# Optimization experiments

Hardware: AMD Instinct MI355X
Metric: run time of the kernel (lower is better)

The kernel has to match this reference:

```python
import jax, jax.numpy as jnp
import numpy as np

B, S, D, H, F = 2, 2048, 1024, 16, 4096
HD = D // H
EPS = 1e-5
NEG = -1e9


def _layernorm(x, g, b):
    mu = jnp.mean(x, axis=-1, keepdims=True)
    var = jnp.mean((x - mu) ** 2, axis=-1, keepdims=True)
    return (x - mu) * jax.lax.rsqrt(var + EPS) * g + b


def _attention(x, wq, wk, wv, wo, bo):
    b, s, d = x.shape
    q = (x @ wq).reshape(b, s, H, HD).transpose(0, 2, 1, 3)  # [b,h,s,hd]
    k = (x @ wk).reshape(b, s, H, HD).transpose(0, 2, 1, 3)
    v = (x @ wv).reshape(b, s, H, HD).transpose(0, 2, 1, 3)
    scores = jnp.einsum('bhqd,bhkd->bhqk', q, k) / (HD ** 0.5)
    # Faithful to source bug: masked_fill(mask == 0, -1e9) where mask = triu(diag=1)
    # -> positions with k <= q (lower triangle incl. diagonal) are filled with -1e9.
    lower = jnp.tril(jnp.ones((s, s), dtype=bool))
    scores = jnp.where(lower, NEG, scores)
    w = jax.nn.softmax(scores, axis=-1)
    o = jnp.einsum('bhqk,bhkd->bhqd', w, v)
    o = o.transpose(0, 2, 1, 3).reshape(b, s, d)
    return o @ wo + bo


def _ffn(x, w1, b1, w2, b2):
    return jax.nn.gelu(x @ w1 + b1, approximate=False) @ w2 + b2


def setup_inputs() -> dict:
    key = jax.random.key(0)
    ks = jax.random.split(key, 10)
    s = 0.02
    return {
        'x': jax.random.normal(ks[0], (B, S, D), jnp.float32),
        'wq': jax.random.normal(ks[1], (D, D), jnp.float32) * s,
        'wk': jax.random.normal(ks[2], (D, D), jnp.float32) * s,
        'wv': jax.random.normal(ks[3], (D, D), jnp.float32) * s,
        'wo': jax.random.normal(ks[4], (D, D), jnp.float32) * s,
        'bo': jnp.zeros((D,), jnp.float32),
        'ln1_g': jnp.ones((D,), jnp.float32),
        'ln1_b': jnp.zeros((D,), jnp.float32),
        'ln2_g': jnp.ones((D,), jnp.float32),
        'ln2_b': jnp.zeros((D,), jnp.float32),
        'w1': jax.random.normal(ks[5], (D, F), jnp.float32) * s,
        'b1': jnp.zeros((F,), jnp.float32),
        'w2': jax.random.normal(ks[6], (F, D), jnp.float32) * s,
        'b2': jnp.zeros((D,), jnp.float32),
    }


def reference(x, wq, wk, wv, wo, bo, ln1_g, ln1_b, ln2_g, ln2_b, w1, b1, w2, b2):
    shortcut = x
    h = _layernorm(x, ln1_g, ln1_b)
    h = _attention(h, wq, wk, wv, wo, bo)  # dropout = identity (eval)
    h = h + shortcut
    shortcut = h
    h2 = _layernorm(h, ln2_g, ln2_b)
    h2 = _attention(h2, wq, wk, wv, wo, bo)  # same attn module reused, per source
    h2 = _ffn(h2, w1, b1, w2, b2)
    return h2 + shortcut
```

## Files before the change

### kernel.cpp

```cpp
#include <hip/hip_runtime.h>
#include <hip/hip_bf16.h>
#include <math.h>

#define Bz 2
#define Sz 2048
#define Dz 1024
#define Hz 16
#define HDz 64
#define Fz 4096
#define ROWS (Bz*Sz)
#define EPSf 1e-5f
#define NEGf -1e9f

typedef __attribute__((ext_vector_type(8))) short short8;
typedef __attribute__((ext_vector_type(4))) float floatx4;

__device__ __forceinline__ unsigned short f2bf(float f){
  __hip_bfloat16 h = __float2bfloat16(f);
  return *(unsigned short*)&h;
}
__device__ __forceinline__ float bf2f(unsigned short u){
  union { unsigned x; float f; } a; a.x = ((unsigned)u) << 16; return a.f;
}

__device__ __forceinline__ float fast_gelu(float x){
  float t  = fabsf(x) * 0.70710678118654752f;
  float kk = __builtin_amdgcn_rcpf(1.0f + 0.3275911f * t);
  float poly = ((((1.061405429f*kk - 1.453152027f)*kk + 1.421413741f)*kk
                 - 0.284496736f)*kk + 0.254829592f)*kk;
  float er = 1.0f - poly * __expf(-t*t);
  er = copysignf(er, x);
  return 0.5f * x * (1.0f + er);
}

__device__ __forceinline__ void gload16(const void* g, void* l){
  __builtin_amdgcn_global_load_lds(
      (const __attribute__((address_space(1))) unsigned int*)g,
      (__attribute__((address_space(3))) unsigned int*)l, 16, 0, 0);
}

__device__ __forceinline__ void xcd_remap(int& bmblk, int& bnblk){
  int gx = gridDim.x, gy = gridDim.y;
  int id = blockIdx.y * gx + blockIdx.x;
  int xcd = id & 7, local = id >> 3;
  bnblk = local % gx;
  bmblk = xcd * (gy >> 3) + local / gx;
}

__global__ __launch_bounds__(256)
void transpose_cast(const float* __restrict__ W, unsigned short* __restrict__ Wt,
                    int K, int N)
{
  __shared__ unsigned short Ts[32][33];
  int n0 = blockIdx.x*32, k0 = blockIdx.y*32;
  int r = threadIdx.x >> 3, c0 = (threadIdx.x & 7) * 4;
  float4 w4 = *(const float4*)(W + (size_t)(k0+r)*N + n0 + c0);
  Ts[r][c0+0] = f2bf(w4.x); Ts[r][c0+1] = f2bf(w4.y);
  Ts[r][c0+2] = f2bf(w4.z); Ts[r][c0+3] = f2bf(w4.w);
  __syncthreads();
  unsigned v0 = Ts[c0+0][r], v1 = Ts[c0+1][r], v2 = Ts[c0+2][r], v3 = Ts[c0+3][r];
  uint2 p; p.x = v0 | (v1<<16); p.y = v2 | (v3<<16);
  *(uint2*)(Wt + (size_t)(n0+r)*K + k0 + c0) = p;
}

__global__ __launch_bounds__(256)
void ln_kernel(const float* __restrict__ in, const float* __restrict__ gam,
               const float* __restrict__ bet, unsigned short* __restrict__ out)
{
  int row = blockIdx.x, t = threadIdx.x;
  size_t base = (size_t)row * Dz;
  int c0 = t * 4;
  float4 x4 = *(const float4*)(in + base + c0);
  float v[4] = {x4.x, x4.y, x4.z, x4.w};
  float s = v[0]+v[1]+v[2]+v[3];
  #pragma unroll
  for (int off=32; off>0; off>>=1) s += __shfl_down(s, off, 64);
  __shared__ float ws[4];
  int lane = t & 63, wid = t >> 6;
  if (lane == 0) ws[wid] = s;
  __syncthreads();
  float mu = (ws[0]+ws[1]+ws[2]+ws[3]) * (1.0f/Dz);
  __syncthreads();
  float d0=v[0]-mu, d1=v[1]-mu, d2=v[2]-mu, d3=v[3]-mu;
  float s2 = d0*d0+d1*d1+d2*d2+d3*d3;
  #pragma unroll
  for (int off=32; off>0; off>>=1) s2 += __shfl_down(s2, off, 64);
  if (lane == 0) ws[wid] = s2;
  __syncthreads();
  float var = (ws[0]+ws[1]+ws[2]+ws[3]) * (1.0f/Dz);
  float rstd = rsqrtf(var + EPSf);
  float4 g4 = *(const float4*)(gam + c0);
  float4 b4 = *(const float4*)(bet + c0);
  unsigned r0 = f2bf((v[0]-mu)*rstd*g4.x + b4.x);
  unsigned r1 = f2bf((v[1]-mu)*rstd*g4.y + b4.y);
  unsigned r2 = f2bf((v[2]-mu)*rstd*g4.z + b4.z);
  unsigned r3 = f2bf((v[3]-mu)*rstd*g4.w + b4.w);
  uint2 p; p.x = r0 | (r1<<16); p.y = r2 | (r3<<16);
  *(uint2*)(out + base + c0) = p;
}

__global__ __launch_bounds__(256)
void gemm_mfma(const unsigned short* __restrict__ A,
               const unsigned short* __restrict__ Bt,
               const float* __restrict__ bias, const float* __restrict__ res,
               float* __restrict__ outf, unsigned short* __restrict__ outb,
               int M, int N, int K, int act, int qkvmode)
{
  __shared__ unsigned short As[2][128*32];
  __shared__ unsigned short Bs[2][128*32];
  int t = threadIdx.x;
  int bmblk, bnblk; xcd_remap(bmblk, bnblk);
  int bm = bmblk * 128, bn = bnblk * 128;
  int wave = t >> 6, lane = t & 63;
  int l15 = lane & 15, quad = lane >> 4;
  int wm = (wave & 1) * 64, wn = (wave >> 1) * 64;
  int srow = wave*32 + (lane >> 2);
  int scbg = ((lane & 3) ^ ((lane >> 3) & 3)) * 8;
  const unsigned short* gA = A  + (size_t)(bm + srow)*K + scbg;
  const unsigned short* gB = Bt + (size_t)(bn + srow)*K + scbg;

  floatx4 acc[4][4];
  #pragma unroll
  for (int i=0;i<4;i++)
    #pragma unroll
    for (int j=0;j<4;j++) acc[i][j] = (floatx4){0.f,0.f,0.f,0.f};

  int swa = ((l15 >> 1) & 3);

  {
    unsigned short* lA = &As[0][wave*32*32];
    unsigned short* lB = &Bs[0][wave*32*32];
    gload16(gA,                lA);
    gload16(gA + (size_t)16*K, lA + 16*32);
    gload16(gB,                lB);
    gload16(gB + (size_t)16*K, lB + 16*32);
  }

  int nIter = K >> 5;
  for (int it = 0; it < nIter; ++it) {
    __syncthreads();
    int cur = it & 1;
    if (it + 1 < nIter) {
      int k1 = (it+1) << 5;
      unsigned short* lA = &As[cur^1][wave*32*32];
      unsigned short* lB = &Bs[cur^1][wave*32*32];
      gload16(gA + k1,                lA);
      gload16(gA + k1 + (size_t)16*K, lA + 16*32);
      gload16(gB + k1,                lB);
      gload16(gB + k1 + (size_t)16*K, lB + 16*32);
    }
    const unsigned short* Ac = As[cur];
    const unsigned short* Bc = Bs[cur];
    short8 af[4], bf[4];
    #pragma unroll
    for (int i=0;i<4;i++) af[i] = *(const short8*)&Ac[(wm + i*16 + l15)*32 + (quad ^ swa)*8];
    #pragma unroll
    for (int j=0;j<4;j++) bf[j] = *(const short8*)&Bc[(wn + j*16 + l15)*32 + (quad ^ swa)*8];
    #pragma unroll
    for (int i=0;i<4;i++)
      #pragma unroll
      for (int j=0;j<4;j++)
        acc[i][j] = __builtin_amdgcn_mfma_f32_16x16x32_bf16(af[i], bf[j], acc[i][j], 0, 0, 0);
  }

  float bj[4];
  #pragma unroll
  for (int j=0;j<4;j++) bj[j] = bias ? bias[bn + wn + j*16 + l15] : 0.f;

  size_t selbase = 0; int ncol = N;
  if (qkvmode) { selbase = (size_t)(bn >> 10) * ((size_t)ROWS * 1024); ncol = 1024; }
  int bnl = qkvmode ? (bn & 1023) : bn;

  #pragma unroll
  for (int i=0;i<4;i++){
    int row0 = bm + wm + i*16 + quad*4;
    #pragma unroll
    for (int r=0;r<4;r++){
      size_t rowoff = selbase + (size_t)(row0 + r) * ncol;
      #pragma unroll
      for (int j=0;j<4;j++){
        float v = acc[i][j][r] + bj[j];
        if (act) v = fast_gelu(v);
        size_t off = rowoff + bnl + wn + j*16 + l15;
        if (res) v += res[off];
        if (outf) outf[off] = v;
        else      outb[off] = f2bf(v);
      }
    }
  }
}

__global__ __launch_bounds__(256)
void gemm_n64(const unsigned short* __restrict__ A,
              const unsigned short* __restrict__ Bt,
              const float* __restrict__ bias, const float* __restrict__ res,
              float* __restrict__ outf, unsigned short* __restrict__ outb,
              int M, int N, int K)
{
  __shared__ unsigned short As[2][128*64];
  __shared__ unsigned short Bs[2][64*64];
  int t = threadIdx.x;
  int bmblk, bnblk; xcd_remap(bmblk, bnblk);
  int bm = bmblk * 128, bn = bnblk * 64;
  int wave = t >> 6, lane = t & 63;
  int l15 = lane & 15, quad = lane >> 4;
  int arow = lane >> 3;
  int acbg = ((lane & 7) ^ arow) * 8;
  const unsigned short* gA = A  + (size_t)(bm + wave*32 + arow)*K + acbg;
  const unsigned short* gB = Bt + (size_t)(bn + wave*16 + arow)*K + acbg;

  floatx4 acc[2][4];
  #pragma unroll
  for (int i=0;i<2;i++)
    #pragma unroll
    for (int j=0;j<4;j++) acc[i][j] = (floatx4){0.f,0.f,0.f,0.f};

  int swr = (l15 & 7);

  {
    unsigned short* lA = &As[0][wave*32*64];
    unsigned short* lB = &Bs[0][wave*16*64];
    gload16(gA,                 lA);
    gload16(gA + (size_t)8*K,   lA + 8*64);
    gload16(gA + (size_t)16*K,  lA + 16*64);
    gload16(gA + (size_t)24*K,  lA + 24*64);
    gload16(gB,                 lB);
    gload16(gB + (size_t)8*K,   lB + 8*64);
  }

  int nIter = K >> 6;
  for (int it = 0; it < nIter; ++it) {
    __syncthreads();
    int cur = it & 1;
    if (it + 1 < nIter) {
      int k1 = (it+1) << 6;
      unsigned short* lA = &As[cur^1][wave*32*64];
      unsigned short* lB = &Bs[cur^1][wave*16*64];
      gload16(gA + k1,                 lA);
      gload16(gA + k1 + (size_t)8*K,   lA + 8*64);
      gload16(gA + k1 + (size_t)16*K,  lA + 16*64);
      gload16(gA + k1 + (size_t)24*K,  lA + 24*64);
      gload16(gB + k1,                 lB);
      gload16(gB + k1 + (size_t)8*K,   lB + 8*64);
    }
    const unsigned short* Ac = As[cur];
    const unsigned short* Bc = Bs[cur];
    #pragma unroll
    for (int ks=0; ks<2; ++ks){
      short8 af[2], bf[4];
      #pragma unroll
      for (int i=0;i<2;i++)
        af[i] = *(const short8*)&Ac[(wave*32 + i*16 + l15)*64 + ((ks*4 + quad) ^ swr)*8];
      #pragma unroll
      for (int j=0;j<4;j++)
        bf[j] = *(const short8*)&Bc[(j*16 + l15)*64 + ((ks*4 + quad) ^ swr)*8];
      #pragma unroll
      for (int i=0;i<2;i++)
        #pragma unroll
        for (int j=0;j<4;j++)
          acc[i][j] = __builtin_amdgcn_mfma_f32_16x16x32_bf16(af[i], bf[j], acc[i][j], 0, 0, 0);
    }
  }

  float bj[4];
  #pragma unroll
  for (int j=0;j<4;j++) bj[j] = bias ? bias[bn + j*16 + l15] : 0.f;

  #pragma unroll
  for (int i=0;i<2;i++){
    int row0 = bm + wave*32 + i*16 + quad*4;
    #pragma unroll
    for (int r=0;r<4;r++){
      size_t rowoff = (size_t)(row0 + r) * N;
      #pragma unroll
      for (int j=0;j<4;j++){
        float v = acc[i][j][r] + bj[j];
        size_t off = rowoff + bn + j*16 + l15;
        if (res) v += res[off];
        if (outf) outf[off] = v;
        else      outb[off] = f2bf(v);
      }
    }
  }
}

__global__ __launch_bounds__(256)
void vmean_kernel(const unsigned short* __restrict__ v, float* __restrict__ vm)
{
  int h = blockIdx.x, b = blockIdx.y;
  int t = threadIdx.x, d = t & 63, seg = t >> 6;
  float s = 0.f;
  for (int i=0;i<512;i++){
    int srow = seg*512 + i;
    s += bf2f(v[((size_t)(b*Sz + srow))*Dz + h*HDz + d]);
  }
  __shared__ float red[4][64];
  red[seg][d] = s;
  __syncthreads();
  if (seg == 0){
    float tot = red[0][d]+red[1][d]+red[2][d]+red[3][d];
    vm[(b*Hz + h)*HDz + d] = tot * (1.0f/2048.0f);
  }
}

__global__ __launch_bounds__(256)
void attn_mfma(const unsigned short* __restrict__ Qg,
               const unsigned short* __restrict__ Kg,
               const unsigned short* __restrict__ Vg,
               const float* __restrict__ vmean,
               unsigned short* __restrict__ Og)
{
  __shared__ unsigned short Ks[128][72];
  __shared__ unsigned short Vts[64][136];
  __shared__ unsigned short Ps[128][72];

  int t = threadIdx.x;
  int wave = t >> 6, lane = t & 63;
  int l15 = lane & 15, quad = lane >> 4;
  int b = blockIdx.z, h = blockIdx.y;
  int qt = b ? (15 - (int)blockIdx.x) : (int)blockIdx.x;

  {
    int r = t >> 1, c = (t & 1) * 32;
    const unsigned short* qp = Qg + ((size_t)(b*Sz + qt*128 + r))*Dz + h*HDz + c;
    uint4 q0 = *(const uint4*)(qp);
    uint4 q1 = *(const uint4*)(qp + 8);
    uint4 q2 = *(const uint4*)(qp + 16);
    uint4 q3 = *(const uint4*)(qp + 24);
    *(uint4*)&Ps[r][c]      = q0;
    *(uint4*)&Ps[r][c + 8]  = q1;
    *(uint4*)&Ps[r][c + 16] = q2;
    *(uint4*)&Ps[r][c + 24] = q3;
  }
  __syncthreads();
  short8 aq[2][2];
  #pragma unroll
  for (int i=0;i<2;i++)
    #pragma unroll
    for (int ks=0;ks<2;ks++)
      aq[i][ks] = *(const short8*)&Ps[wave*32 + i*16 + l15][ks*32 + quad*8];

  floatx4 acc_o[2][4];
  #pragma unroll
  for (int i=0;i<2;i++)
    #pragma unroll
    for (int j=0;j<4;j++) acc_o[i][j] = (floatx4){0.f,0.f,0.f,0.f};
  float lacc[2][4];
  #pragma unroll
  for (int i=0;i<2;i++)
    #pragma unroll
    for (int r=0;r<4;r++) lacc[i][r] = 0.f;

  int sr = t >> 2, sc = (t & 3) * 16;

  uint4 pk0,pk1,pk2,pk3,pv0,pv1,pv2,pv3;
  {
    size_t off0 = ((size_t)(b*Sz + qt*128 + sr))*Dz + h*HDz + sc;
    size_t off1 = off0 + (size_t)64*Dz;
    pk0 = *(const uint4*)(Kg + off0); pk1 = *(const uint4*)(Kg + off0 + 8);
    pk2 = *(const uint4*)(Kg + off1); pk3 = *(const uint4*)(Kg + off1 + 8);
    pv0 = *(const uint4*)(Vg + off0); pv1 = *(const uint4*)(Vg + off0 + 8);
    pv2 = *(const uint4*)(Vg + off1); pv3 = *(const uint4*)(Vg + off1 + 8);
  }

  for (int jt2 = qt; jt2 < Sz/128; ++jt2) {
    __syncthreads();
    {
      *(uint4*)&Ks[sr][sc]        = pk0; *(uint4*)&Ks[sr][sc + 8]      = pk1;
      *(uint4*)&Ks[64 + sr][sc]   = pk2; *(uint4*)&Ks[64 + sr][sc + 8] = pk3;
      unsigned short e[16];
      e[0]=pv0.x&0xffff; e[1]=pv0.x>>16; e[2]=pv0.y&0xffff; e[3]=pv0.y>>16;
      e[4]=pv0.z&0xffff; e[5]=pv0.z>>16; e[6]=pv0.w&0xffff; e[7]=pv0.w>>16;
      e[8]=pv1.x&0xffff; e[9]=pv1.x>>16; e[10]=pv1.y&0xffff; e[11]=pv1.y>>16;
      e[12]=pv1.z&0xffff; e[13]=pv1.z>>16; e[14]=pv1.w&0xffff; e[15]=pv1.w>>16;
      #pragma unroll
      for (int j=0;j<16;j++) Vts[sc + j][sr] = e[j];
      e[0]=pv2.x&0xffff; e[1]=pv2.x>>16; e[2]=pv2.y&0xffff; e[3]=pv2.y>>16;
      e[4]=pv2.z&0xffff; e[5]=pv2.z>>16; e[6]=pv2.w&0xffff; e[7]=pv2.w>>16;
      e[8]=pv3.x&0xffff; e[9]=pv3.x>>16; e[10]=pv3.y&0xffff; e[11]=pv3.y>>16;
      e[12]=pv3.z&0xffff; e[13]=pv3.z>>16; e[14]=pv3.w&0xffff; e[15]=pv3.w>>16;
      #pragma unroll
      for (int j=0;j<16;j++) Vts[sc + j][64 + sr] = e[j];
    }
    __syncthreads();

    if (jt2 + 1 < Sz/128) {
      size_t off0 = ((size_t)(b*Sz + (jt2+1)*128 + sr))*Dz + h*HDz + sc;
      size_t off1 = off0 + (size_t)64*Dz;
      pk0 = *(const uint4*)(Kg + off0); pk1 = *(const uint4*)(Kg + off0 + 8);
      pk2 = *(const uint4*)(Kg + off1); pk3 = *(const uint4*)(Kg + off1 + 8);
      pv0 = *(const uint4*)(Vg + off0); pv1 = *(const uint4*)(Vg + off0 + 8);
      pv2 = *(const uint4*)(Vg + off1); pv3 = *(const uint4*)(Vg + off1 + 8);
    }

    #pragma unroll
    for (int hh=0; hh<2; ++hh){
      floatx4 acc_s[2][4];
      #pragma unroll
      for (int i=0;i<2;i++)
        #pragma unroll
        for (int j=0;j<4;j++) acc_s[i][j] = (floatx4){0.f,0.f,0.f,0.f};
      #pragma unroll
      for (int ks=0;ks<2;ks++){
        short8 bk[4];
        #pragma unroll
        for (int j=0;j<4;j++) bk[j] = *(const short8*)&Ks[hh*64 + j*16 + l15][ks*32 + quad*8];
        #pragma unroll
        for (int i=0;i<2;i++)
          #pragma unroll
          for (int j=0;j<4;j++)
            acc_s[i][j] = __builtin_amdgcn_mfma_f32_16x16x32_bf16(aq[i][ks], bk[j], acc_s[i][j], 0, 0, 0);
      }
      #pragma unroll
      for (int i=0;i<2;i++){
        #pragma unroll
        for (int j=0;j<4;j++){
          int kj = jt2*128 + hh*64 + j*16 + l15;
          #pragma unroll
          for (int r=0;r<4;r++){
            int qrow = qt*128 + wave*32 + i*16 + quad*4 + r;
            float s = acc_s[i][j][r] * 0.125f;
            if (kj <= qrow) s = NEGf;
            float p = __expf(fminf(s, 80.f));
            lacc[i][r] += p;
            Ps[wave*32 + i*16 + quad*4 + r][j*16 + l15] = f2bf(p);
          }
        }
      }
      #pragma unroll
      for (int ks=0;ks<2;ks++){
        short8 ap[2], bv[4];
        #pragma unroll
        for (int i=0;i<2;i++) ap[i] = *(const short8*)&Ps[wave*32 + i*16 + l15][ks*32 + quad*8];
        #pragma unroll
        for (int j=0;j<4;j++) bv[j] = *(const short8*)&Vts[j*16 + l15][hh*64 + ks*32 + quad*8];
        #pragma unroll
        for (int i=0;i<2;i++)
          #pragma unroll
          for (int j=0;j<4;j++)
            acc_o[i][j] = __builtin_amdgcn_mfma_f32_16x16x32_bf16(ap[i], bv[j], acc_o[i][j], 0, 0, 0);
      }
    }
  }

  #pragma unroll
  for (int i=0;i<2;i++){
    #pragma unroll
    for (int r=0;r<4;r++){
      float l = lacc[i][r];
      l += __shfl_xor(l, 1, 64);
      l += __shfl_xor(l, 2, 64);
      l += __shfl_xor(l, 4, 64);
      l += __shfl_xor(l, 8, 64);
      int qrow = qt*128 + wave*32 + i*16 + quad*4 + r;
      float inv = 1.0f / l;
      size_t rowoff = ((size_t)(b*Sz + qrow))*Dz + h*HDz;
      #pragma unroll
      for (int j=0;j<4;j++){
        float ov = acc_o[i][j][r] * inv;
        if (qrow == Sz-1) ov = vmean[(b*Hz + h)*HDz + j*16 + l15];
        Og[rowoff + j*16 + l15] = f2bf(ov);
      }
    }
  }
}

extern "C" void kernel_launch(void* const* d_in, const int* in_sizes, int n_in,
                              void* d_out, int out_size, void* d_ws, size_t ws_size,
                              hipStream_t stream)
{
  const float* x    = (const float*)d_in[0];
  const float* wq   = (const float*)d_in[1];
  const float* wk   = (const float*)d_in[2];
  const float* wv   = (const float*)d_in[3];
  const float* wo   = (const float*)d_in[4];
  const float* bo   = (const float*)d_in[5];
  const float* ln1g = (const float*)d_in[6];
  const float* ln1b = (const float*)d_in[7];
  const float* ln2g = (const float*)d_in[8];
  const float* ln2b = (const float*)d_in[9];
  const float* w1   = (const float*)d_in[10];
  const float* b1   = (const float*)d_in[11];
  const float* w2   = (const float*)d_in[12];
  const float* b2   = (const float*)d_in[13];
  float* out = (float*)d_out;

  const size_t MB = 1024*1024;
  char* w = (char*)d_ws;
  float*          trunk = (float*)(w);
  unsigned short* lnb   = (unsigned short*)(w + 16*MB);
  float*          vmean = (float*)(w + 16*MB);
  unsigned short* q     = (unsigned short*)(w + 24*MB);
  unsigned short* k     = (unsigned short*)(w + 32*MB);
  unsigned short* v     = (unsigned short*)(w + 40*MB);
  unsigned short* ctx   = (unsigned short*)(w + 48*MB);
  unsigned short* wqkvT = (unsigned short*)(w + 56*MB);
  unsigned short* wqT   = wqkvT;
  unsigned short* wkT   = (unsigned short*)(w + 58*MB);
  unsigned short* wvT   = (unsigned short*)(w + 60*MB);
  unsigned short* woT   = (unsigned short*)(w + 62*MB);
  unsigned short* w1T   = (unsigned short*)(w + 64*MB);
  unsigned short* w2T   = (unsigned short*)(w + 72*MB);
  unsigned short* mid   = (unsigned short*)(w + 24*MB);

  dim3 blk(256);
  transpose_cast<<<dim3(32,32),  blk, 0, stream>>>(wq, wqT, Dz, Dz);
  transpose_cast<<<dim3(32,32),  blk, 0, stream>>>(wk, wkT, Dz, Dz);
  transpose_cast<<<dim3(32,32),  blk, 0, stream>>>(wv, wvT, Dz, Dz);
  transpose_cast<<<dim3(32,32),  blk, 0, stream>>>(wo, woT, Dz, Dz);
  transpose_cast<<<dim3(128,32), blk, 0, stream>>>(w1, w1T, Dz, Fz);
  transpose_cast<<<dim3(32,128), blk, 0, stream>>>(w2, w2T, Fz, Dz);

  dim3 gln(ROWS);
  dim3 gqkv(3*Dz/128, ROWS/128);
  dim3 gn64(Dz/64,  ROWS/128);
  dim3 gf1(Fz/128, ROWS/128);
  dim3 gattn(Sz/128, Hz, Bz);
  dim3 gvm(Hz, Bz);

  ln_kernel<<<gln, blk, 0, stream>>>(x, ln1g, ln1b, lnb);
  gemm_mfma<<<gqkv, blk, 0, stream>>>(lnb, wqkvT, nullptr, nullptr, nullptr, q, ROWS, 3*Dz, Dz, 0, 1);
  vmean_kernel<<<gvm, blk, 0, stream>>>(v, vmean);
  attn_mfma<<<gattn, blk, 0, stream>>>(q, k, v, vmean, ctx);
  gemm_n64<<<gn64, blk, 0, stream>>>(ctx, woT, bo, x, trunk, nullptr, ROWS, Dz, Dz);

  ln_kernel<<<gln, blk, 0, stream>>>(trunk, ln2g, ln2b, lnb);
  gemm_mfma<<<gqkv, blk, 0, stream>>>(lnb, wqkvT, nullptr, nullptr, nullptr, q, ROWS, 3*Dz, Dz, 0, 1);
  vmean_kernel<<<gvm, blk, 0, stream>>>(v, vmean);
  attn_mfma<<<gattn, blk, 0, stream>>>(q, k, v, vmean, ctx);
  gemm_n64<<<gn64, blk, 0, stream>>>(ctx, woT, bo, nullptr, nullptr, lnb, ROWS, Dz, Dz);
  gemm_mfma<<<gf1, blk, 0, stream>>>(lnb, w1T, b1, nullptr, nullptr, mid, ROWS, Fz, Dz, 1, 0);
  gemm_n64<<<gn64, blk, 0, stream>>>(mid, w2T, b2, trunk, out, nullptr, ROWS, Dz, Fz);
}
```

Baseline: 531.8 us.

## Replace 128x128 GEMM with 256x256 8-wave pipelined kernel and split-K FFN2

Replaces the 128x128 bf16 MFMA GEMM with a 256x256-tile, 512-thread kernel that uses a K-tile of 64, XOR-swizzled LDS, and an interleaved schedule of staged loads, barriers and prioritized MFMA phases. It is used for the QKV and FFN1 projections. When the workspace is large enough, FFN2 runs as a 4-way split-K with this kernel, followed by a reduction kernel that adds bias and residual. The aim is more operand reuse per tile and better overlap of loads with MFMA work, at the cost of fewer blocks (possible wave quantization), higher register pressure, and extra memory traffic for the split-K partials.

```diff
diff --git a/kernel.cpp b/kernel.cpp
--- a/kernel.cpp
+++ b/kernel.cpp
@@ -38,6 +38,15 @@
       (const __attribute__((address_space(1))) unsigned int*)g,
       (__attribute__((address_space(3))) unsigned int*)l, 16, 0, 0);
 }
+
+__device__ __forceinline__ void bar(){
+  asm volatile("" ::: "memory");
+  __builtin_amdgcn_s_barrier();
+  asm volatile("" ::: "memory");
+}
+#define WAITV6 asm volatile("s_waitcnt vmcnt(6)" ::: "memory")
+#define WAITV0 asm volatile("s_waitcnt vmcnt(0)" ::: "memory")
+#define WL0    asm volatile("s_waitcnt lgkmcnt(0)" ::: "memory")
 
 __device__ __forceinline__ void xcd_remap(int& bmblk, int& bnblk){
   int gx = gridDim.x, gy = gridDim.y;
@@ -99,81 +108,176 @@
   *(uint2*)(out + base + c0) = p;
 }
 
-__global__ __launch_bounds__(256)
-void gemm_mfma(const unsigned short* __restrict__ A,
-               const unsigned short* __restrict__ Bt,
-               const float* __restrict__ bias, const float* __restrict__ res,
-               float* __restrict__ outf, unsigned short* __restrict__ outb,
-               int M, int N, int K, int act, int qkvmode)
-{
-  __shared__ unsigned short As[2][128*32];
-  __shared__ unsigned short Bs[2][128*32];
+#define STG_A(buf, half, k0) { \
+  _Pragma("unroll") for (int c_=0;c_<2;c_++){ \
+    int sg_ = c_*8 + wave; \
+    int row0_ = ((sg_>>3)<<7) + ((sg_&7)<<3) + ((half)<<6); \
+    gload16(pA[half][c_] + (k0), &As[buf][row0_*64]); } }
+
+#define STG_B(buf, jh, k0) { \
+  _Pragma("unroll") for (int c_=0;c_<2;c_++){ \
+    int sg_ = c_*8 + wave; int rho0_ = sg_<<3; \
+    gload16(pB[jh][c_] + (k0), &Bs[buf][jh][rho0_*64]); } }
+
+#define READ_A4(dst, buf, ihalf) { \
+  _Pragma("unroll") for (int ii_=0; ii_<4; ++ii_){ \
+    int row_ = wm*128 + ((ihalf)*4+ii_)*16 + l15; \
+    _Pragma("unroll") for (int ks_=0; ks_<2; ++ks_){ \
+      int slot_ = (ks_*4+quad) ^ (l15&7); \
+      dst[ii_][ks_] = *(const short8*)&As[buf][row_*64 + slot_*8]; } } }
+
+#define READ_B2(dst, buf, jh) { \
+  _Pragma("unroll") for (int jl_=0; jl_<2; ++jl_){ \
+    int rho_ = wn*32 + jl_*16 + l15; \
+    _Pragma("unroll") for (int ks_=0; ks_<2; ++ks_){ \
+      int slot_ = (ks_*4+quad) ^ (l15&7); \
+      dst[jl_][ks_] = *(const short8*)&Bs[buf][jh][rho_*64 + slot_*8]; } } }
+
+#define MFMA_PH(IH, JH, AF, BF) { \
+  __builtin_amdgcn_s_setprio(1); \
+  _Pragma("unroll") for (int ii_=0; ii_<4; ++ii_){ \
+    _Pragma("unroll") for (int jl_=0; jl_<2; ++jl_){ \
+      floatx4 c_ = acc[(IH)*4+ii_][(JH)*2+jl_]; \
+      c_ = __builtin_amdgcn_mfma_f32_16x16x32_bf16(AF[ii_][0], BF[jl_][0], c_, 0,0,0); \
+      c_ = __builtin_amdgcn_mfma_f32_16x16x32_bf16(AF[ii_][1], BF[jl_][1], c_, 0,0,0); \
+      acc[(IH)*4+ii_][(JH)*2+jl_] = c_; } } \
+  __builtin_amdgcn_s_setprio(0); }
+
+__global__ __launch_bounds__(512, 2)
+void gemm256(const unsigned short* __restrict__ A,
+             const unsigned short* __restrict__ Bt,
+             const float* __restrict__ bias, const float* __restrict__ res,
+             float* __restrict__ outf, unsigned short* __restrict__ outb,
+             int M, int N, int K, int lda, int ldb, int act, int qkvmode)
+{
+  __shared__ unsigned short As[2][256*64];
+  __shared__ unsigned short Bs[2][2][128*64];
+
   int t = threadIdx.x;
-  int bmblk, bnblk; xcd_remap(bmblk, bnblk);
-  int bm = bmblk * 128, bn = bnblk * 128;
   int wave = t >> 6, lane = t & 63;
   int l15 = lane & 15, quad = lane >> 4;
-  int wm = (wave & 1) * 64, wn = (wave >> 1) * 64;
-  int srow = wave*32 + (lane >> 2);
-  int scbg = ((lane & 3) ^ ((lane >> 3) & 3)) * 8;
-  const unsigned short* gA = A  + (size_t)(bm + srow)*K + scbg;
-  const unsigned short* gB = Bt + (size_t)(bn + srow)*K + scbg;
-
-  floatx4 acc[4][4];
-  #pragma unroll
-  for (int i=0;i<4;i++)
+  int wm = wave >> 2, wn = wave & 3;
+
+  int nN = gridDim.x, nM = gridDim.y;
+  int id = blockIdx.y * nN + blockIdx.x;
+  int xcd = id & 7, local = id >> 3;
+  int bnblk = local % nN;
+  int bmblk = xcd * (nM >> 3) + local / nN;
+  int bm = bmblk * 256, bn = bnblk * 256;
+
+  if (gridDim.z > 1){
+    A    += (size_t)blockIdx.z * K;
+    Bt   += (size_t)blockIdx.z * K;
+    outf += (size_t)blockIdx.z * ((size_t)M * N);
+  }
+
+  int lrow = lane >> 3;
+  int lcol = ((lane & 7) ^ (lane >> 3)) * 8;
+
+  const unsigned short* pA[2][2];
+  const unsigned short* pB[2][2];
+  #pragma unroll
+  for (int half=0; half<2; half++)
+    #pragma unroll
+    for (int c=0;c<2;c++){
+      int sg = c*8 + wave;
+      int row0 = ((sg>>3)<<7) + ((sg&7)<<3) + (half<<6);
+      pA[half][c] = A + (size_t)(bm + row0 + lrow)*lda + lcol;
+    }
+  #pragma unroll
+  for (int jh=0; jh<2; jh++)
+    #pragma unroll
+    for (int c=0;c<2;c++){
+      int sg = c*8 + wave;
+      int rho0 = sg<<3;
+      int gn = ((rho0>>5)<<6) + (jh<<5) + (rho0&31);
+      pB[jh][c] = Bt + (size_t)(bn + gn + lrow)*ldb + lcol;
+    }
+
+  floatx4 acc[8][4];
+  #pragma unroll
+  for (int i=0;i<8;i++)
     #pragma unroll
     for (int j=0;j<4;j++) acc[i][j] = (floatx4){0.f,0.f,0.f,0.f};
 
-  int swa = ((l15 >> 1) & 3);
-
-  {
-    unsigned short* lA = &As[0][wave*32*32];
-    unsigned short* lB = &Bs[0][wave*32*32];
-    gload16(gA,                lA);
-    gload16(gA + (size_t)16*K, lA + 16*32);
-    gload16(gB,                lB);
-    gload16(gB + (size_t)16*K, lB + 16*32);
-  }
-
-  int nIter = K >> 5;
-  for (int it = 0; it < nIter; ++it) {
-    __syncthreads();
-    int cur = it & 1;
-    if (it + 1 < nIter) {
-      int k1 = (it+1) << 5;
-      unsigned short* lA = &As[cur^1][wave*32*32];
-      unsigned short* lB = &Bs[cur^1][wave*32*32];
-      gload16(gA + k1,                lA);
-      gload16(gA + k1 + (size_t)16*K, lA + 16*32);
-      gload16(gB + k1,                lB);
-      gload16(gB + k1 + (size_t)16*K, lB + 16*32);
-    }
-    const unsigned short* Ac = As[cur];
-    const unsigned short* Bc = Bs[cur];
-    short8 af[4], bf[4];
-    #pragma unroll
-    for (int i=0;i<4;i++) af[i] = *(const short8*)&Ac[(wm + i*16 + l15)*32 + (quad ^ swa)*8];
-    #pragma unroll
-    for (int j=0;j<4;j++) bf[j] = *(const short8*)&Bc[(wn + j*16 + l15)*32 + (quad ^ swa)*8];
-    #pragma unroll
-    for (int i=0;i<4;i++)
-      #pragma unroll
-      for (int j=0;j<4;j++)
-        acc[i][j] = __builtin_amdgcn_mfma_f32_16x16x32_bf16(af[i], bf[j], acc[i][j], 0, 0, 0);
+  STG_A(0, 0, 0);  STG_A(0, 1, 0);
+  STG_B(0, 0, 0);  STG_B(0, 1, 0);
+  STG_A(1, 0, 64); STG_A(1, 1, 64);
+  STG_B(1, 0, 64);
+  WAITV6;
+  bar();
+
+  int NKT = K >> 6;
+  int nIter = NKT >> 1;
+  for (int it = 0; it < nIter; ++it){
+    bool more = (it + 1 < nIter);
+    int k0B  = (2*it+1) << 6;
+    int k0A2 = (2*it+2) << 6;
+    int k0B2 = (2*it+3) << 6;
+    short8 aLo[4][2], aHi[4][2], bcur[2][2];
+
+    READ_A4(aLo, 0, 0);
+    READ_B2(bcur, 0, 0);
+    STG_B(1, 1, k0B);
+    bar(); WL0;
+    MFMA_PH(0, 0, aLo, bcur);
+    bar();
+
+    READ_A4(aHi, 0, 1);
+    READ_B2(bcur, 0, 0);
+    if (more) STG_A(0, 0, k0A2);
+    bar(); WL0;
+    MFMA_PH(1, 0, aHi, bcur);
+    bar();
+
+    READ_B2(bcur, 0, 1);
+    if (more) STG_A(0, 1, k0A2);
+    bar(); WL0;
+    MFMA_PH(0, 1, aLo, bcur);
+    bar();
+
+    if (more) { STG_B(0, 0, k0A2); WAITV6; }
+    else      { WAITV0; }
+    bar();
+    MFMA_PH(1, 1, aHi, bcur);
+    bar();
+
+    READ_A4(aLo, 1, 0);
+    READ_B2(bcur, 1, 0);
+    if (more) STG_B(0, 1, k0A2);
+    bar(); WL0;
+    MFMA_PH(0, 0, aLo, bcur);
+    bar();
+
+    READ_A4(aHi, 1, 1);
+    READ_B2(bcur, 1, 0);
+    if (more) STG_A(1, 0, k0B2);
+    bar(); WL0;
+    MFMA_PH(1, 0, aHi, bcur);
+    bar();
+
+    READ_B2(bcur, 1, 1);
+    if (more) STG_A(1, 1, k0B2);
+    bar(); WL0;
+    MFMA_PH(0, 1, aLo, bcur);
+    bar();
+
+    if (more) { STG_B(1, 0, k0B2); WAITV6; }
+    bar();
+    MFMA_PH(1, 1, aHi, bcur);
+    bar();
   }
 
   float bj[4];
   #pragma unroll
-  for (int j=0;j<4;j++) bj[j] = bias ? bias[bn + wn + j*16 + l15] : 0.f;
-
-  size_t selbase = 0; int ncol = N;
-  if (qkvmode) { selbase = (size_t)(bn >> 10) * ((size_t)ROWS * 1024); ncol = 1024; }
-  int bnl = qkvmode ? (bn & 1023) : bn;
-
-  #pragma unroll
-  for (int i=0;i<4;i++){
-    int row0 = bm + wm + i*16 + quad*4;
+  for (int j=0;j<4;j++) bj[j] = bias ? bias[bn + wn*64 + j*16 + l15] : 0.f;
+
+  size_t selbase = 0; int ncol = N; int bnl = bn;
+  if (qkvmode){ selbase = (size_t)(bn >> 10) * ((size_t)M * 1024); ncol = 1024; bnl = bn & 1023; }
+
+  #pragma unroll
+  for (int i=0;i<8;i++){
+    int row0 = bm + wm*128 + i*16 + quad*4;
     #pragma unroll
     for (int r=0;r<4;r++){
       size_t rowoff = selbase + (size_t)(row0 + r) * ncol;
@@ -181,7 +285,7 @@
       for (int j=0;j<4;j++){
         float v = acc[i][j][r] + bj[j];
         if (act) v = fast_gelu(v);
-        size_t off = rowoff + bnl + wn + j*16 + l15;
+        size_t off = rowoff + bnl + wn*64 + j*16 + l15;
         if (res) v += res[off];
         if (outf) outf[off] = v;
         else      outb[off] = f2bf(v);
@@ -282,6 +386,27 @@
       }
     }
   }
+}
+
+__global__ __launch_bounds__(256)
+void reduce4(const float* __restrict__ part, const float* __restrict__ bias,
+             const float* __restrict__ res, float* __restrict__ out)
+{
+  const size_t NN = (size_t)ROWS * Dz;
+  size_t i = ((size_t)blockIdx.x * 256 + threadIdx.x) * 4;
+  float4 a = *(const float4*)(part + i);
+  float4 b = *(const float4*)(part + NN + i);
+  float4 c = *(const float4*)(part + 2*NN + i);
+  float4 d = *(const float4*)(part + 3*NN + i);
+  float4 r = *(const float4*)(res + i);
+  int col = threadIdx.x * 4;
+  float4 g = *(const float4*)(bias + col);
+  float4 o;
+  o.x = a.x+b.x+c.x+d.x + g.x + r.x;
+  o.y = a.y+b.y+c.y+d.y + g.y + r.y;
+  o.z = a.z+b.z+c.z+d.z + g.z + r.z;
+  o.w = a.w+b.w+c.w+d.w + g.w + r.w;
+  *(float4*)(out + i) = o;
 }
 
 __global__ __launch_bounds__(256)
@@ -502,8 +627,10 @@
   unsigned short* w1T   = (unsigned short*)(w + 64*MB);
   unsigned short* w2T   = (unsigned short*)(w + 72*MB);
   unsigned short* mid   = (unsigned short*)(w + 24*MB);
-
-  dim3 blk(256);
+  float*          part  = (float*)(w + 80*MB);
+  bool splitk = ws_size >= (size_t)144*MB;
+
+  dim3 blk(256), blk512(512);
   transpose_cast<<<dim3(32,32),  blk, 0, stream>>>(wq, wqT, Dz, Dz);
   transpose_cast<<<dim3(32,32),  blk, 0, stream>>>(wk, wkT, Dz, Dz);
   transpose_cast<<<dim3(32,32),  blk, 0, stream>>>(wv, wvT, Dz, Dz);
@@ -512,23 +639,28 @@
   transpose_cast<<<dim3(32,128), blk, 0, stream>>>(w2, w2T, Fz, Dz);
 
   dim3 gln(ROWS);
-  dim3 gqkv(3*Dz/128, ROWS/128);
+  dim3 gqkv(3*Dz/256, ROWS/256);
+  dim3 gf1(Fz/256,  ROWS/256);
   dim3 gn64(Dz/64,  ROWS/128);
-  dim3 gf1(Fz/128, ROWS/128);
   dim3 gattn(Sz/128, Hz, Bz);
   dim3 gvm(Hz, Bz);
 
   ln_kernel<<<gln, blk, 0, stream>>>(x, ln1g, ln1b, lnb);
-  gemm_mfma<<<gqkv, blk, 0, stream>>>(lnb, wqkvT, nullptr, nullptr, nullptr, q, ROWS, 3*Dz, Dz, 0, 1);
+  gemm256<<<gqkv, blk512, 0, stream>>>(lnb, wqkvT, nullptr, nullptr, nullptr, q, ROWS, 3*Dz, Dz, Dz, Dz, 0, 1);
   vmean_kernel<<<gvm, blk, 0, stream>>>(v, vmean);
   attn_mfma<<<gattn, blk, 0, stream>>>(q, k, v, vmean, ctx);
   gemm_n64<<<gn64, blk, 0, stream>>>(ctx, woT, bo, x, trunk, nullptr, ROWS, Dz, Dz);
 
   ln_kernel<<<gln, blk, 0, stream>>>(trunk, ln2g, ln2b, lnb);
-  gemm_mfma<<<gqkv, blk, 0, stream>>>(lnb, wqkvT, nullptr, nullptr, nullptr, q, ROWS, 3*Dz, Dz, 0, 1);
+  gemm256<<<gqkv, blk512, 0, stream>>>(lnb, wqkvT, nullptr, nullptr, nullptr, q, ROWS, 3*Dz, Dz, Dz, Dz, 0, 1);
   vmean_kernel<<<gvm, blk, 0, stream>>>(v, vmean);
   attn_mfma<<<gattn, blk, 0, stream>>>(q, k, v, vmean, ctx);
   gemm_n64<<<gn64, blk, 0, stream>>>(ctx, woT, bo, nullptr, nullptr, lnb, ROWS, Dz, Dz);
-  gemm_mfma<<<gf1, blk, 0, stream>>>(lnb, w1T, b1, nullptr, nullptr, mid, ROWS, Fz, Dz, 1, 0);
-  gemm_n64<<<gn64, blk, 0, stream>>>(mid, w2T, b2, trunk, out, nullptr, ROWS, Dz, Fz);
-}
+  gemm256<<<gf1, blk512, 0, stream>>>(lnb, w1T, b1, nullptr, nullptr, mid, ROWS, Fz, Dz, Dz, Dz, 1, 0);
+  if (splitk) {
+    gemm256<<<dim3(4,16,4), blk512, 0, stream>>>(mid, w2T, nullptr, nullptr, part, nullptr, ROWS, Dz, Fz/4, Fz, Fz, 0, 0);
+    reduce4<<<dim3(4096), blk, 0, stream>>>(part, b2, trunk, out);
+  } else {
+    gemm_n64<<<gn64, blk, 0, stream>>>(mid, w2T, b2, trunk, out, nullptr, ROWS, Dz, Fz);
+  }
+}
```

Measured after the change: 540.1 us. No clear change (+1.6%).
